# Kernel tuning notes

Measured on AMD Instinct MI355X. Metric: run time of the kernel, lower is better.

## Reference

```python
import jax, jax.numpy as jnp
import numpy as np

EMBED_DIM = 1280
NUM_HEADS = 16
HEAD_DIM = EMBED_DIM // NUM_HEADS  # 80
SCALE = HEAD_DIM ** -0.5
BATCH = 16
SEQ = 1024


def setup_inputs() -> dict:
    key = jax.random.key(0)
    k1, k2, k3, k4, k5 = jax.random.split(key, 5)
    return {
        "hidden_states": jax.random.normal(k1, (BATCH, SEQ, EMBED_DIM), dtype=jnp.float32),
        "w_qkv": jax.random.normal(k2, (EMBED_DIM, 3 * EMBED_DIM), dtype=jnp.float32) * (EMBED_DIM ** -0.5),
        "b_qkv": jax.random.normal(k3, (3 * EMBED_DIM,), dtype=jnp.float32) * 0.02,
        "w_proj": jax.random.normal(k4, (EMBED_DIM, EMBED_DIM), dtype=jnp.float32) * (EMBED_DIM ** -0.5),
        "b_proj": jax.random.normal(k5, (EMBED_DIM,), dtype=jnp.float32) * 0.02,
    }


def reference(hidden_states, w_qkv, b_qkv, w_proj, b_proj):
    b, s, e = hidden_states.shape
    # QKV projection: [b, s, 3e] -> [3, b, h, s, d]
    qkv = hidden_states @ w_qkv + b_qkv
    qkv = qkv.reshape(b, s, 3, NUM_HEADS, HEAD_DIM).transpose(2, 0, 3, 1, 4)
    q, k, v = qkv[0], qkv[1], qkv[2]
    # full attention matrix [b, h, s, s]
    attn = jnp.einsum("bhqd,bhkd->bhqk", q, k) * SCALE
    attn = jax.nn.softmax(attn, axis=-1)
    # dropout p=0.0 (eval): identity
    out = jnp.einsum("bhqk,bhkd->bhqd", attn, v)
    out = out.transpose(0, 2, 1, 3).reshape(b, s, e)
    return out @ w_proj + b_proj
```

## Files before the change

### kernel.cpp

```cpp
#include <hip/hip_runtime.h>

#define BATCH 16
#define SEQ   1024
#define EMBED 1280
#define NH    16
#define HD    80
#define HDP   96
#define NQKV  3840
#define MTOK  (BATCH*SEQ)
#define SCALE 0.11180339887498948f
#define LOG2E 1.4426950408889634f

#define SK_STRIDE 104
#define SV_STRIDE 72
#define SP_STRIDE 72

typedef _Float16 half8 __attribute__((ext_vector_type(8)));
typedef _Float16 half4 __attribute__((ext_vector_type(4)));
typedef float floatx4 __attribute__((ext_vector_type(4)));

#define GLD_TO_LDS(gp, lp)                                                        \
  __builtin_amdgcn_global_load_lds(                                               \
      (const __attribute__((address_space(1))) void*)(gp),                        \
      (__attribute__((address_space(3))) void*)(lp), 16, 0, 0)

__device__ __forceinline__ float rowmax16(float x) {
#define DPP_MAX(ctrl)                                                             \
  {                                                                               \
    float y = __int_as_float(                                                     \
        __builtin_amdgcn_update_dpp(0, __float_as_int(x), ctrl, 0xF, 0xF, true)); \
    x = fmaxf(x, y);                                                              \
  }
  DPP_MAX(0xB1);
  DPP_MAX(0x4E);
  DPP_MAX(0x141);
  DPP_MAX(0x140);
#undef DPP_MAX
  return x;
}

__global__ void cvt_f32_to_f16(const float4* __restrict__ in, _Float16* __restrict__ out, int n4) {
  int i = blockIdx.x * blockDim.x + threadIdx.x;
  if (i < n4) {
    float4 v = in[i];
    half4 h;
    h[0] = (_Float16)v.x; h[1] = (_Float16)v.y; h[2] = (_Float16)v.z; h[3] = (_Float16)v.w;
    *(half4*)(out + (size_t)i * 4) = h;
  }
}

template <int N>
__global__ void cvt_transpose_f16(const float* __restrict__ in, _Float16* __restrict__ out) {
  __shared__ float tile[32][33];
  const int tx = threadIdx.x & 31, ty = threadIdx.x >> 5;
  const int k0 = blockIdx.y * 32;
  const int n0 = blockIdx.x * 32;
#pragma unroll
  for (int j = 0; j < 4; ++j)
    tile[ty + 8 * j][tx] = in[(size_t)(k0 + ty + 8 * j) * N + n0 + tx];
  __syncthreads();
#pragma unroll
  for (int j = 0; j < 4; ++j)
    out[(size_t)(n0 + ty + 8 * j) * 1280 + k0 + tx] = (_Float16)tile[tx][ty + 8 * j];
}


#define STAGE_A(H, T, D)                                                           \
  do {                                                                             \
    GLD_TO_LDS(aSrc0 + (size_t)((H) * 128) * 1280 + (T) * 64,                      \
               &sA[D][((H) * 128 + wave * 16) * 64]);                              \
    GLD_TO_LDS(aSrc0 + (size_t)((H) * 128 + 8) * 1280 + (T) * 64,                  \
               &sA[D][((H) * 128 + wave * 16 + 8) * 64]);                          \
  } while (0)

#define STAGE_B(H, T, D)                                                           \
  do {                                                                             \
    GLD_TO_LDS(bSrc0 + (size_t)((H) * 128) * 1280 + (T) * 64,                      \
               &sB[D][((H) * 128 + wave * 16) * 64]);                              \
    GLD_TO_LDS(bSrc0 + (size_t)((H) * 128 + 8) * 1280 + (T) * 64,                  \
               &sB[D][((H) * 128 + wave * 16 + 8) * 64]);                          \
  } while (0)

#define LDS_FRAG(P, ROWB, FR, KK) (*(const half8*)((P) + ((ROWB) + (FR) * 16) * 64 + cofs[KK]))

#define MFMA_Q(MIB, NIB)                                                           \
  _Pragma("unroll") for (int mi = 0; mi < 4; ++mi)                                 \
    _Pragma("unroll") for (int ni = 0; ni < 2; ++ni)                               \
      _Pragma("unroll") for (int kk = 0; kk < 2; ++kk)                             \
        acc[(MIB) + mi][(NIB) + ni] = __builtin_amdgcn_mfma_f32_16x16x32_f16(      \
            af[mi][kk], bf[(NIB) + ni][kk], acc[(MIB) + mi][(NIB) + ni], 0, 0, 0)

#define GBODY(T, D, S1, S2, VNSTR)                                                 \
  {                                                                                \
    const _Float16* pA = &sA[D][0];                                                \
    const _Float16* pB = &sB[D][0];                                                \
                         \
    _Pragma("unroll") for (int mi = 0; mi < 4; ++mi)                               \
      _Pragma("unroll") for (int kk = 0; kk < 2; ++kk)                             \
        af[mi][kk] = LDS_FRAG(pA, rA, mi, kk);                                     \
    _Pragma("unroll") for (int ni = 0; ni < 2; ++ni)                               \
      _Pragma("unroll") for (int kk = 0; kk < 2; ++kk)                             \
        bf[ni][kk] = LDS_FRAG(pB, rB, ni, kk);                                     \
    if (S1) { STAGE_A(1, (T) + 1, (D) ^ 1); }                                      \
    __builtin_amdgcn_s_setprio(1);                                                 \
    MFMA_Q(0, 0);                                                                  \
    __builtin_amdgcn_s_setprio(0);                                                 \
    __builtin_amdgcn_s_barrier();                                                  \
                                                   \
    _Pragma("unroll") for (int ni = 0; ni < 2; ++ni)                               \
      _Pragma("unroll") for (int kk = 0; kk < 2; ++kk)                             \
        bf[2 + ni][kk] = LDS_FRAG(pB, rB, 2 + ni, kk);                             \
    __builtin_amdgcn_s_setprio(1);                                                 \
    MFMA_Q(0, 2);                                                                  \
    __builtin_amdgcn_s_setprio(0);                                                 \
    __builtin_amdgcn_s_barrier();                                                  \
                                  \
    _Pragma("unroll") for (int mi = 0; mi < 4; ++mi)                               \
      _Pragma("unroll") for (int kk = 0; kk < 2; ++kk)                             \
        af[mi][kk] = LDS_FRAG(pA, rA, 4 + mi, kk);                                 \
    if (S2) { STAGE_B(0, (T) + 2, (D)); }                                          \
    __builtin_amdgcn_s_setprio(1);                                                 \
    MFMA_Q(4, 0);                                                                  \
    __builtin_amdgcn_s_setprio(0);                                                 \
    __builtin_amdgcn_s_barrier();                                                  \
                 \
    if (S2) { STAGE_A(0, (T) + 2, (D)); STAGE_B(1, (T) + 2, (D)); }                \
    __builtin_amdgcn_s_setprio(1);                                                 \
    MFMA_Q(4, 2);                                                                  \
    __builtin_amdgcn_s_setprio(0);                                                 \
    asm volatile("s_waitcnt " VNSTR ::: "memory");                                 \
    __builtin_amdgcn_s_barrier();                                                  \
  }

template <int MODE>
__global__ __launch_bounds__(512, 2)
void gemm256(const _Float16* __restrict__ A, const _Float16* __restrict__ Bt,
             const float* __restrict__ bias,
             _Float16* __restrict__ q_pad, _Float16* __restrict__ k_pad,
             _Float16* __restrict__ v_t, float* __restrict__ outf) {
  __shared__ __align__(16) _Float16 sA[2][256 * 64];
  __shared__ __align__(16) _Float16 sB[2][256 * 64];

  const int tid = threadIdx.x;
  const int wave = tid >> 6, lane = tid & 63, quad = lane >> 4, r16 = lane & 15;
  const int wm = wave >> 2, wn = wave & 3;

  const int pid = blockIdx.x;
  const int xcd = pid & 7, local = pid >> 3;
  const int mt = xcd * 8 + (local & 7);
  const int nt = local >> 3;
  const int m0 = mt * 256, n0 = nt * 256;

  const int l8 = lane >> 3, cg = (lane & 7) ^ l8;
  const _Float16* aSrc0 = A + ((size_t)m0 + wave * 16 + l8) * 1280 + cg * 8;
  const _Float16* bSrc0 = Bt + ((size_t)n0 + wave * 16 + l8) * 1280 + cg * 8;

  const int rA = wm * 128 + r16;
  const int rB = wn * 64 + r16;
  const int cofs[2] = { ((0 + quad) ^ (r16 & 7)) * 8, ((4 + quad) ^ (r16 & 7)) * 8 };

  floatx4 acc[8][4] = {};
  half8 af[4][2], bf[4][2];

  STAGE_A(0, 0, 0); STAGE_A(1, 0, 0); STAGE_B(0, 0, 0); STAGE_B(1, 0, 0);
  STAGE_B(0, 1, 1); STAGE_A(0, 1, 1); STAGE_B(1, 1, 1);
  asm volatile("s_waitcnt vmcnt(6)" ::: "memory");
  __builtin_amdgcn_s_barrier();

  for (int it = 0; it < 9; ++it) {
    GBODY(2 * it, 0, true, true, "vmcnt(6)");
    GBODY(2 * it + 1, 1, true, true, "vmcnt(6)");
  }
  GBODY(18, 0, true, false, "vmcnt(0)");
  GBODY(19, 1, false, false, "vmcnt(0)");

  if (MODE == 1) {
#pragma unroll
    for (int mi = 0; mi < 8; ++mi)
#pragma unroll
      for (int ni = 0; ni < 4; ++ni) {
        int n = n0 + wn * 64 + ni * 16 + r16;
        float bv = bias[n];
#pragma unroll
        for (int r = 0; r < 4; ++r) {
          int m = m0 + wm * 128 + mi * 16 + quad * 4 + r;
          outf[(size_t)m * EMBED + n] = acc[mi][ni][r] + bv;
        }
      }
  } else {
#pragma unroll
    for (int mi = 0; mi < 8; ++mi)
#pragma unroll
      for (int ni = 0; ni < 4; ++ni) {
        int n = n0 + wn * 64 + ni * 16 + r16;
        float bv = bias[n];
        int which = n / 1280;
        int rem = n - which * 1280;
        int h = rem / 80;
        int d = rem - h * 80;
#pragma unroll
        for (int r = 0; r < 4; ++r) {
          int m = m0 + wm * 128 + mi * 16 + quad * 4 + r;
          int b = m >> 10, s = m & 1023;
          int bh = b * NH + h;
          _Float16 val = (_Float16)(acc[mi][ni][r] + bv);
          if (which == 0) {
            q_pad[((size_t)bh * SEQ + s) * HDP + d] = val;
            if (d < 16) q_pad[((size_t)bh * SEQ + s) * HDP + 80 + d] = (_Float16)0.f;
          } else if (which == 1) {
            k_pad[((size_t)bh * SEQ + s) * HDP + d] = val;
            if (d < 16) k_pad[((size_t)bh * SEQ + s) * HDP + 80 + d] = (_Float16)0.f;
          } else {
            v_t[((size_t)bh * HD + d) * SEQ + s] = val;
          }
        }
      }
  }
}

__global__ __launch_bounds__(256, 2)
void attn_kernel(const _Float16* __restrict__ q_pad, const _Float16* __restrict__ k_pad,
                 const _Float16* __restrict__ v_t, _Float16* __restrict__ attn_out) {
  __shared__ __align__(16) _Float16 sK[2][64 * SK_STRIDE];
  __shared__ __align__(16) _Float16 sV[2][96 * SV_STRIDE];
  __shared__ __align__(16) _Float16 sP[4][16 * SP_STRIDE];

  const int tid = threadIdx.x;
  const int wave = tid >> 6, lane = tid & 63, quad = lane >> 4, r16 = lane & 15;
  const int bh = blockIdx.x >> 3;
  const int q0 = (blockIdx.x & 7) * 128;

  if (tid < 128) {
    int row = 80 + (tid >> 3), col = (tid & 7) * 8;
    half8 z;
#pragma unroll
    for (int j = 0; j < 8; ++j) z[j] = (row == 80) ? (_Float16)1.f : (_Float16)0.f;
    *(half8*)(&sV[0][row * SV_STRIDE + col]) = z;
    *(half8*)(&sV[1][row * SV_STRIDE + col]) = z;
  }

  half8 qf[2][3];
#pragma unroll
  for (int mi = 0; mi < 2; ++mi) {
    const _Float16* qb = q_pad + ((size_t)bh * SEQ + q0 + wave * 32 + mi * 16 + r16) * HDP;
#pragma unroll
    for (int kq = 0; kq < 3; ++kq) {
      half8 q = *(const half8*)(qb + kq * 32 + quad * 8);
#pragma unroll
      for (int j = 0; j < 8; ++j) q[j] = q[j] * (_Float16)(SCALE * LOG2E);
      qf[mi][kq] = q;
    }
  }

  int rowK[3], colK[3];
#pragma unroll
  for (int i = 0; i < 3; ++i) {
    int c = tid + i * 256;
    rowK[i] = c / 12; colK[i] = c - rowK[i] * 12;
  }
  const int rowV0 = tid >> 3, colV0 = tid & 7;
  const _Float16* kgb = k_pad + ((size_t)bh * SEQ) * HDP;
  const _Float16* vgb = v_t + (size_t)bh * HD * SEQ;

  {
    uint4 tk0 = *(const uint4*)(kgb + (size_t)(rowK[0]) * HDP + colK[0] * 8);
    uint4 tk1 = *(const uint4*)(kgb + (size_t)(rowK[1]) * HDP + colK[1] * 8);
    uint4 tk2 = *(const uint4*)(kgb + (size_t)(rowK[2]) * HDP + colK[2] * 8);
    uint4 tv0 = *(const uint4*)(vgb + (size_t)(rowV0) * SEQ + colV0 * 8);
    uint4 tv1 = *(const uint4*)(vgb + (size_t)(rowV0 + 32) * SEQ + colV0 * 8);
    *(uint4*)(&sK[0][rowK[0] * SK_STRIDE + colK[0] * 8]) = tk0;
    *(uint4*)(&sK[0][rowK[1] * SK_STRIDE + colK[1] * 8]) = tk1;
    *(uint4*)(&sK[0][rowK[2] * SK_STRIDE + colK[2] * 8]) = tk2;
    *(uint4*)(&sV[0][(rowV0)*SV_STRIDE + colV0 * 8]) = tv0;
    *(uint4*)(&sV[0][(rowV0 + 32) * SV_STRIDE + colV0 * 8]) = tv1;
    if (tid < 128) {
      uint4 tv2 = *(const uint4*)(vgb + (size_t)(rowV0 + 64) * SEQ + colV0 * 8);
      *(uint4*)(&sV[0][(rowV0 + 64) * SV_STRIDE + colV0 * 8]) = tv2;
    }
  }

  floatx4 o[2][6] = {};
  float mrow[2][4];
#pragma unroll
  for (int mi = 0; mi < 2; ++mi)
#pragma unroll
    for (int r = 0; r < 4; ++r) mrow[mi][r] = -1e30f;

  __syncthreads();

  for (int kt = 0; kt < 16; ++kt) {
    const int cur = kt & 1, nxt = cur ^ 1;

    uint4 tk0, tk1, tk2, tv0, tv1, tv2;
    if (kt < 15) {
      const int kb = (kt + 1) * 64;
      tk0 = *(const uint4*)(kgb + (size_t)(kb + rowK[0]) * HDP + colK[0] * 8);
      tk1 = *(const uint4*)(kgb + (size_t)(kb + rowK[1]) * HDP + colK[1] * 8);
      tk2 = *(const uint4*)(kgb + (size_t)(kb + rowK[2]) * HDP + colK[2] * 8);
      tv0 = *(const uint4*)(vgb + (size_t)(rowV0)*SEQ + kb + colV0 * 8);
      tv1 = *(const uint4*)(vgb + (size_t)(rowV0 + 32) * SEQ + kb + colV0 * 8);
      if (tid < 128)
        tv2 = *(const uint4*)(vgb + (size_t)(rowV0 + 64) * SEQ + kb + colV0 * 8);
    }

    floatx4 sacc[2][4] = {};
    __builtin_amdgcn_s_setprio(1);
#pragma unroll
    for (int ni = 0; ni < 4; ++ni)
#pragma unroll
      for (int kq = 0; kq < 3; ++kq) {
        half8 kf = *(const half8*)(&sK[cur][(ni * 16 + r16) * SK_STRIDE + kq * 32 + quad * 8]);
#pragma unroll
        for (int mi = 0; mi < 2; ++mi)
          sacc[mi][ni] = __builtin_amdgcn_mfma_f32_16x16x32_f16(qf[mi][kq], kf, sacc[mi][ni], 0, 0, 0);
      }
    __builtin_amdgcn_s_setprio(0);

    if (kt < 15) {
      *(uint4*)(&sK[nxt][rowK[0] * SK_STRIDE + colK[0] * 8]) = tk0;
      *(uint4*)(&sK[nxt][rowK[1] * SK_STRIDE + colK[1] * 8]) = tk1;
      *(uint4*)(&sK[nxt][rowK[2] * SK_STRIDE + colK[2] * 8]) = tk2;
      *(uint4*)(&sV[nxt][(rowV0)*SV_STRIDE + colV0 * 8]) = tv0;
      *(uint4*)(&sV[nxt][(rowV0 + 32) * SV_STRIDE + colV0 * 8]) = tv1;
      if (tid < 128)
        *(uint4*)(&sV[nxt][(rowV0 + 64) * SV_STRIDE + colV0 * 8]) = tv2;
    }

#pragma unroll
    for (int mi = 0; mi < 2; ++mi)
#pragma unroll
      for (int r = 0; r < 4; ++r) {
        float mx = fmaxf(fmaxf(sacc[mi][0][r], sacc[mi][1][r]),
                         fmaxf(sacc[mi][2][r], sacc[mi][3][r]));
        mx = rowmax16(mx);
        float mnew = fmaxf(mrow[mi][r], mx);
        float alpha = __builtin_amdgcn_exp2f(mrow[mi][r] - mnew);
        mrow[mi][r] = mnew;
#pragma unroll
        for (int ni = 0; ni < 4; ++ni)
          sacc[mi][ni][r] = __builtin_amdgcn_exp2f(sacc[mi][ni][r] - mnew);
#pragma unroll
        for (int di = 0; di < 6; ++di) o[mi][di][r] *= alpha;
      }

#pragma unroll
    for (int mi = 0; mi < 2; ++mi) {
#pragma unroll
      for (int ni = 0; ni < 4; ++ni)
#pragma unroll
        for (int r = 0; r < 4; ++r)
          sP[wave][(quad * 4 + r) * SP_STRIDE + ni * 16 + r16] = (_Float16)sacc[mi][ni][r];
#pragma unroll
      for (int kp = 0; kp < 2; ++kp) {
        half8 pf = *(const half8*)(&sP[wave][r16 * SP_STRIDE + kp * 32 + quad * 8]);
        __builtin_amdgcn_s_setprio(1);
#pragma unroll
        for (int di = 0; di < 6; ++di) {
          half8 vf = *(const half8*)(&sV[cur][(di * 16 + r16) * SV_STRIDE + kp * 32 + quad * 8]);
          o[mi][di] = __builtin_amdgcn_mfma_f32_16x16x32_f16(pf, vf, o[mi][di], 0, 0, 0);
        }
        __builtin_amdgcn_s_setprio(0);
      }
    }

    __syncthreads();
  }

  const int b = bh >> 4, h = bh & 15;
#pragma unroll
  for (int mi = 0; mi < 2; ++mi)
#pragma unroll
    for (int r = 0; r < 4; ++r) {
      float l = __shfl(o[mi][5][r], lane & 48);
      float inv = 1.0f / l;
      int tok = b * SEQ + q0 + wave * 32 + mi * 16 + quad * 4 + r;
#pragma unroll
      for (int di = 0; di < 5; ++di) {
        int e = h * HD + di * 16 + r16;
        attn_out[(size_t)tok * EMBED + e] = (_Float16)(o[mi][di][r] * inv);
      }
    }
}

extern "C" void kernel_launch(void* const* d_in, const int* in_sizes, int n_in,
                              void* d_out, int out_size, void* d_ws, size_t ws_size,
                              hipStream_t stream) {
  const float* hidden = (const float*)d_in[0];
  const float* w_qkv  = (const float*)d_in[1];
  const float* b_qkv  = (const float*)d_in[2];
  const float* w_proj = (const float*)d_in[3];
  const float* b_proj = (const float*)d_in[4];
  float* out = (float*)d_out;

  char* ws = (char*)d_ws;
  size_t off = 0;
  _Float16* hidden_h = (_Float16*)(ws + off); off += (size_t)MTOK * EMBED * 2;
  _Float16* wqkv_t   = (_Float16*)(ws + off); off += (size_t)NQKV * EMBED * 2;
  _Float16* wproj_t  = (_Float16*)(ws + off); off += (size_t)EMBED * EMBED * 2;
  _Float16* q_pad    = (_Float16*)(ws + off); off += (size_t)BATCH * NH * SEQ * HDP * 2;
  _Float16* k_pad    = (_Float16*)(ws + off); off += (size_t)BATCH * NH * SEQ * HDP * 2;
  _Float16* v_t      = (_Float16*)(ws + off); off += (size_t)BATCH * NH * HD * SEQ * 2;
  _Float16* attn_out = hidden_h;

  {
    int n4 = MTOK * EMBED / 4;
    cvt_f32_to_f16<<<(n4 + 255) / 256, 256, 0, stream>>>((const float4*)hidden, hidden_h, n4);
  }
  cvt_transpose_f16<NQKV><<<dim3(NQKV / 32, 1280 / 32), 256, 0, stream>>>(w_qkv, wqkv_t);
  cvt_transpose_f16<EMBED><<<dim3(EMBED / 32, 1280 / 32), 256, 0, stream>>>(w_proj, wproj_t);

  gemm256<0><<<960, 512, 0, stream>>>(hidden_h, wqkv_t, b_qkv, q_pad, k_pad, v_t, nullptr);

  attn_kernel<<<BATCH * NH * (SEQ / 128), 256, 0, stream>>>(q_pad, k_pad, v_t, attn_out);

  gemm256<1><<<320, 512, 0, stream>>>(attn_out, wproj_t, b_proj, nullptr, nullptr, nullptr, out);
}
```

Baseline: 627.1 us.

## Restructure GEMM main loop prefetch schedule and vectorize V transpose stores

Reworks the GEMM k-loop body so all four B fragments load at once. The A tile for the next step is issued at the start of each iteration and both B halves two steps ahead after a single mid-iteration barrier, cutting barriers from four to two per step and adjusting the vmcnt waits to match. In the QKV epilogue, the four consecutive sequence rows for V are packed into one half4 store instead of four scalar stores. The new schedule changes how much load latency is hidden and raises register pressure from holding all B fragments.

Result: faster. 596.1 us (-4.9%).

```diff
diff --git a/kernel.cpp b/kernel.cpp
--- a/kernel.cpp
+++ b/kernel.cpp
@@ -90,42 +90,28 @@
         acc[(MIB) + mi][(NIB) + ni] = __builtin_amdgcn_mfma_f32_16x16x32_f16(      \
             af[mi][kk], bf[(NIB) + ni][kk], acc[(MIB) + mi][(NIB) + ni], 0, 0, 0)
 
-#define GBODY(T, D, S1, S2, VNSTR)                                                 \
+#define GBODY2(T, D, SA, SB, VNSTR)                                                \
   {                                                                                \
     const _Float16* pA = &sA[D][0];                                                \
     const _Float16* pB = &sB[D][0];                                                \
-                         \
+    if (SA) { STAGE_A(0, (T) + 1, (D) ^ 1); STAGE_A(1, (T) + 1, (D) ^ 1); }        \
     _Pragma("unroll") for (int mi = 0; mi < 4; ++mi)                               \
       _Pragma("unroll") for (int kk = 0; kk < 2; ++kk)                             \
         af[mi][kk] = LDS_FRAG(pA, rA, mi, kk);                                     \
-    _Pragma("unroll") for (int ni = 0; ni < 2; ++ni)                               \
+    _Pragma("unroll") for (int ni = 0; ni < 4; ++ni)                               \
       _Pragma("unroll") for (int kk = 0; kk < 2; ++kk)                             \
         bf[ni][kk] = LDS_FRAG(pB, rB, ni, kk);                                     \
-    if (S1) { STAGE_A(1, (T) + 1, (D) ^ 1); }                                      \
     __builtin_amdgcn_s_setprio(1);                                                 \
     MFMA_Q(0, 0);                                                                  \
-    __builtin_amdgcn_s_setprio(0);                                                 \
-    __builtin_amdgcn_s_barrier();                                                  \
-                                                   \
-    _Pragma("unroll") for (int ni = 0; ni < 2; ++ni)                               \
-      _Pragma("unroll") for (int kk = 0; kk < 2; ++kk)                             \
-        bf[2 + ni][kk] = LDS_FRAG(pB, rB, 2 + ni, kk);                             \
-    __builtin_amdgcn_s_setprio(1);                                                 \
     MFMA_Q(0, 2);                                                                  \
     __builtin_amdgcn_s_setprio(0);                                                 \
-    __builtin_amdgcn_s_barrier();                                                  \
-                                  \
     _Pragma("unroll") for (int mi = 0; mi < 4; ++mi)                               \
       _Pragma("unroll") for (int kk = 0; kk < 2; ++kk)                             \
         af[mi][kk] = LDS_FRAG(pA, rA, 4 + mi, kk);                                 \
-    if (S2) { STAGE_B(0, (T) + 2, (D)); }                                          \
+    __builtin_amdgcn_s_barrier();                                                  \
+    if (SB) { STAGE_B(0, (T) + 2, (D)); STAGE_B(1, (T) + 2, (D)); }                \
     __builtin_amdgcn_s_setprio(1);                                                 \
     MFMA_Q(4, 0);                                                                  \
-    __builtin_amdgcn_s_setprio(0);                                                 \
-    __builtin_amdgcn_s_barrier();                                                  \
-                 \
-    if (S2) { STAGE_A(0, (T) + 2, (D)); STAGE_B(1, (T) + 2, (D)); }                \
-    __builtin_amdgcn_s_setprio(1);                                                 \
     MFMA_Q(4, 2);                                                                  \
     __builtin_amdgcn_s_setprio(0);                                                 \
     asm volatile("s_waitcnt " VNSTR ::: "memory");                                 \
@@ -163,16 +149,16 @@
   half8 af[4][2], bf[4][2];
 
   STAGE_A(0, 0, 0); STAGE_A(1, 0, 0); STAGE_B(0, 0, 0); STAGE_B(1, 0, 0);
-  STAGE_B(0, 1, 1); STAGE_A(0, 1, 1); STAGE_B(1, 1, 1);
-  asm volatile("s_waitcnt vmcnt(6)" ::: "memory");
+  STAGE_B(0, 1, 1); STAGE_B(1, 1, 1);
+  asm volatile("s_waitcnt vmcnt(4)" ::: "memory");
   __builtin_amdgcn_s_barrier();
 
   for (int it = 0; it < 9; ++it) {
-    GBODY(2 * it, 0, true, true, "vmcnt(6)");
-    GBODY(2 * it + 1, 1, true, true, "vmcnt(6)");
-  }
-  GBODY(18, 0, true, false, "vmcnt(0)");
-  GBODY(19, 1, false, false, "vmcnt(0)");
+    GBODY2(2 * it, 0, true, true, "vmcnt(4)");
+    GBODY2(2 * it + 1, 1, true, true, "vmcnt(4)");
+  }
+  GBODY2(18, 0, true, false, "vmcnt(0)");
+  GBODY2(19, 1, false, false, "vmcnt(0)");
 
   if (MODE == 1) {
 #pragma unroll
@@ -198,20 +184,21 @@
         int rem = n - which * 1280;
         int h = rem / 80;
         int d = rem - h * 80;
-#pragma unroll
-        for (int r = 0; r < 4; ++r) {
-          int m = m0 + wm * 128 + mi * 16 + quad * 4 + r;
-          int b = m >> 10, s = m & 1023;
-          int bh = b * NH + h;
-          _Float16 val = (_Float16)(acc[mi][ni][r] + bv);
-          if (which == 0) {
-            q_pad[((size_t)bh * SEQ + s) * HDP + d] = val;
-            if (d < 16) q_pad[((size_t)bh * SEQ + s) * HDP + 80 + d] = (_Float16)0.f;
-          } else if (which == 1) {
-            k_pad[((size_t)bh * SEQ + s) * HDP + d] = val;
-            if (d < 16) k_pad[((size_t)bh * SEQ + s) * HDP + 80 + d] = (_Float16)0.f;
-          } else {
-            v_t[((size_t)bh * HD + d) * SEQ + s] = val;
+        int mbase = m0 + wm * 128 + mi * 16 + quad * 4;
+        int b = mbase >> 10, s = mbase & 1023;
+        int bh = b * NH + h;
+        if (which == 2) {
+          half4 pv;
+#pragma unroll
+          for (int r = 0; r < 4; ++r) pv[r] = (_Float16)(acc[mi][ni][r] + bv);
+          *(half4*)(v_t + ((size_t)bh * HD + d) * SEQ + s) = pv;
+        } else {
+          _Float16* dst = (which == 0) ? q_pad : k_pad;
+#pragma unroll
+          for (int r = 0; r < 4; ++r) {
+            _Float16 val = (_Float16)(acc[mi][ni][r] + bv);
+            dst[((size_t)bh * SEQ + (s + r)) * HDP + d] = val;
+            if (d < 16) dst[((size_t)bh * SEQ + (s + r)) * HDP + 80 + d] = (_Float16)0.f;
           }
         }
       }
```
